# Performance work log

Hardware: AMD Instinct MI355X
Metric: run time of the kernel (lower is better)

The kernel has to match this reference:

```python
import jax, jax.numpy as jnp
import numpy as np

NUM_ROUTES, NUM_TIME, DIM, K, C = 100000, 2016, 256, 100, 5
BATCH = 262144


def _xavier(key, shape):
    fan_in, fan_out = shape[0], shape[1]
    lim = np.sqrt(6.0 / (fan_in + fan_out))
    return jax.random.uniform(key, shape, jnp.float32, -lim, lim)


def setup_inputs() -> dict:
    key = jax.random.key(0)
    ks = jax.random.split(key, 9)
    route_idx = jax.random.randint(ks[0], (BATCH,), 0, NUM_ROUTES)
    time_idx = jax.random.randint(ks[1], (BATCH,), 0, NUM_TIME)
    route_table = _xavier(ks[2], (NUM_ROUTES, DIM))
    time_table = _xavier(ks[3], (NUM_TIME, DIM))
    w = _xavier(ks[4], (DIM, K))
    mode_a = _xavier(ks[5], (DIM, C))
    mode_b = _xavier(ks[6], (DIM, C))
    mode_bias = jnp.zeros((C, C), jnp.float32)
    fc_lim = 1.0 / np.sqrt(C * C + K)
    fc_w = jax.random.uniform(ks[7], (C * C + K, 1), jnp.float32, -fc_lim, fc_lim)
    fc_b = jax.random.uniform(ks[8], (1,), jnp.float32, -fc_lim, fc_lim)
    return {
        "route_idx": route_idx, "time_idx": time_idx,
        "route_table": route_table, "time_table": time_table,
        "w": w, "mode_a": mode_a, "mode_b": mode_b,
        "mode_bias": mode_bias, "fc_w": fc_w, "fc_b": fc_b,
    }


def reference(route_idx, time_idx, route_table, time_table, w, mode_a, mode_b, mode_bias, fc_w, fc_b):
    r = route_table[route_idx]            # [B, D]
    t = time_table[time_idx]              # [B, D]
    gcp = jax.nn.relu((r * t) @ w)        # [B, K]
    # einsum('ni,nj->nij') then contracting i with mode_a and j with mode_b
    # equals outer product of the two small projections (exact same math):
    ra = r @ mode_a                       # [B, C]
    tb = t @ mode_b                       # [B, C]
    inter = jax.nn.sigmoid(ra[:, :, None] * tb[:, None, :] + mode_bias)  # [B, C, C]
    feats = jnp.concatenate([gcp, inter.reshape(inter.shape[0], -1)], axis=1)  # [B, K + C*C]
    out = feats @ fc_w + fc_b             # [B, 1]
    return jnp.squeeze(out, axis=-1)      # [B]
```

## Files before the change

kernel.cpp:

```cpp
#include <hip/hip_runtime.h>
#include <stdint.h>

#define BATCH   262144
#define NROUTES 100000
#define NTIME   2016
#define DIM     256
#define KOUT    100
#define NTILES  7

typedef __attribute__((ext_vector_type(2))) float f32x2;
typedef __attribute__((ext_vector_type(4))) float f32x4;

#define WS_WFRAG_BYTES ((size_t)(NTILES * 8 * 64 * 8))
#define WS_RA_OFF   (WS_WFRAG_BYTES)
#define WS_TB_OFF   (WS_RA_OFF + (size_t)NROUTES * 32)
#define WS_RT8_OFF  (WS_TB_OFF + (size_t)NTIME * 32)
#define WS_TT8_OFF  (WS_RT8_OFF + (size_t)NROUTES * 256)
#define WS_NEED     (WS_TT8_OFF + (size_t)NTIME * 256)

template<int CTRL>
static __device__ __forceinline__ float dpp_add(float x) {
  int s = __builtin_amdgcn_update_dpp(0, __builtin_bit_cast(int, x), CTRL, 0xF, 0xF, true);
  return x + __builtin_bit_cast(float, s);
}
static __device__ __forceinline__ float wave_sum63(float x) {
  x = dpp_add<0x111>(x);
  x = dpp_add<0x112>(x);
  x = dpp_add<0x114>(x);
  x = dpp_add<0x118>(x);
  x = dpp_add<0x142>(x);
  x = dpp_add<0x143>(x);
  return x;
}
static __device__ __forceinline__ float sum16_all(float x) {
  x = dpp_add<0x0B1>(x);
  x = dpp_add<0x04E>(x);
  x = dpp_add<0x124>(x);
  x = dpp_add<0x128>(x);
  return x;
}
static __device__ __forceinline__ float sigm(float z) {
  return __builtin_amdgcn_rcpf(1.0f + __expf(-z));
}

template<int DO8>
__global__ __launch_bounds__(256) void prep_kernel(
    const float* __restrict__ route_table,
    const float* __restrict__ time_table,
    const float* __restrict__ w,
    const float* __restrict__ mode_a,
    const float* __restrict__ mode_b,
    uint8_t* __restrict__ ws)
{
  const int b   = blockIdx.x;
  const int tid = threadIdx.x;

  if (b < 14) {
    const int u = b * 256 + tid;
    const int lane = u & 63;
    const int frag = u >> 6;
    const int ks = frag / NTILES;
    const int nt = frag % NTILES;
    const int n  = nt * 16 + (lane & 15);
    const int k0 = ks * 32 + (lane >> 4) * 8;
    float v[8];
    #pragma unroll
    for (int j = 0; j < 8; ++j)
      v[j] = (n < KOUT) ? w[(size_t)(k0 + j) * KOUT + n] : 0.0f;
    uint32_t d0 = 0, d1 = 0;
    d0 = __builtin_amdgcn_cvt_pk_fp8_f32(v[0], v[1], d0, false);
    d0 = __builtin_amdgcn_cvt_pk_fp8_f32(v[2], v[3], d0, true);
    d1 = __builtin_amdgcn_cvt_pk_fp8_f32(v[4], v[5], d1, false);
    d1 = __builtin_amdgcn_cvt_pk_fp8_f32(v[6], v[7], d1, true);
    ((uint2*)ws)[u] = make_uint2(d0, d1);
    return;
  }

  const float* tab; const float* proj; float* outp; uint8_t* out8; int base;
  if (b < 14 + 63) {
    tab = time_table;  proj = mode_b; outp = (float*)(ws + WS_TB_OFF);
    out8 = ws + WS_TT8_OFF; base = (b - 14) * 32;
  } else {
    tab = route_table; proj = mode_a; outp = (float*)(ws + WS_RA_OFF);
    out8 = ws + WS_RT8_OFF; base = (b - 77) * 32;
  }

  const int wave = tid >> 6, lane = tid & 63;
  const int perm = (2 * (lane >> 4) + ((lane >> 1) & 1)) * 8 +
                   ((lane >> 2) & 3) * 2 + (lane & 1);

  float A[4][5];
  #pragma unroll
  for (int j = 0; j < 4; ++j)
    #pragma unroll
    for (int i = 0; i < 5; ++i)
      A[j][i] = proj[(4 * perm + j) * 5 + i];

  const int row0 = base + wave * 8;
  float4 v[8];
  #pragma unroll
  for (int rr = 0; rr < 8; ++rr)
    v[rr] = *(const float4*)(tab + (size_t)(row0 + rr) * DIM + 4 * perm);

  #pragma unroll
  for (int rr = 0; rr < 8; ++rr) {
    const int row = row0 + rr;
    if (DO8) {
      uint32_t u = 0;
      u = __builtin_amdgcn_cvt_pk_fp8_f32(8.f * v[rr].x, 8.f * v[rr].y, u, false);
      u = __builtin_amdgcn_cvt_pk_fp8_f32(8.f * v[rr].z, 8.f * v[rr].w, u, true);
      *(uint32_t*)(out8 + (size_t)row * 256 + 4 * lane) = u;
    }
    float p[5];
    #pragma unroll
    for (int i = 0; i < 5; ++i) {
      float s = v[rr].x * A[0][i] + v[rr].y * A[1][i] + v[rr].z * A[2][i] + v[rr].w * A[3][i];
      p[i] = wave_sum63(s);
    }
    if (lane == 63) {
      float* o = outp + (size_t)row * 8;
      *(f32x4*)o = (f32x4){p[0], p[1], p[2], p[3]};
      o[4] = p[4];
    }
  }
}

__global__ __launch_bounds__(256, 3) void main_pipelined(
    const int*   __restrict__ route_idx,
    const int*   __restrict__ time_idx,
    const float* __restrict__ mode_bias,
    const float* __restrict__ fc_w,
    const float* __restrict__ fc_b,
    const uint8_t* __restrict__ ws,
    float* __restrict__ out)
{
  __shared__ uint4 wlds[1792];
  const int tid  = threadIdx.x;
  const int wave = tid >> 6, lane = tid & 63;
  const int col  = lane & 15, quad = lane >> 4;
  const int base = (blockIdx.x * 4 + wave) * 64;

  int ri[4], ti[4];
  #pragma unroll
  for (int t = 0; t < 4; ++t) {
    ri[t] = route_idx[base + t * 16 + col];
    ti[t] = time_idx[base + t * 16 + col];
  }

  {
    const uint4* wsrc = (const uint4*)ws;
    #pragma unroll
    for (int j = 0; j < 7; ++j)
      wlds[j * 256 + tid] = wsrc[j * 256 + tid];
  }

  float fcw_l[NTILES];
  #pragma unroll
  for (int nt = 0; nt < NTILES; ++nt) {
    const int n = nt * 16 + col;
    fcw_l[nt] = (n < KOUT) ? fc_w[n] * 0.015625f : 0.0f;
  }
  const float fb = fc_b[0];

  uint4 rw[2][4], tw[2][4];
  auto issue = [&](int buf, int t) {
    const uint8_t* rb = ws + WS_RT8_OFF + (size_t)ri[t] * 256 + quad * 16;
    const uint8_t* tb = ws + WS_TT8_OFF + (size_t)ti[t] * 256 + quad * 16;
    #pragma unroll
    for (int i = 0; i < 4; ++i) {
      rw[buf][i] = *(const uint4*)(rb + i * 64);
      tw[buf][i] = *(const uint4*)(tb + i * 64);
    }
  };

  issue(0, 0);
  __syncthreads();

  const uint2* wl2 = (const uint2*)wlds;

  #pragma unroll
  for (int it = 0; it < 4; ++it) {
    const int cb = it & 1, nb = cb ^ 1;

    const float* rap = (const float*)(ws + WS_RA_OFF) + (size_t)ri[it] * 8;
    const float* tbp = (const float*)(ws + WS_TB_OFF) + (size_t)ti[it] * 8;
    f32x4 ra0 = *(const f32x4*)rap; float ra4 = rap[4];
    f32x4 tb0 = *(const f32x4*)tbp; float tb4 = tbp[4];
    if (it < 3) issue(nb, it + 1);

    f32x4 acc[NTILES];
    #pragma unroll
    for (int nt = 0; nt < NTILES; ++nt) acc[nt] = (f32x4){0.f, 0.f, 0.f, 0.f};

    #pragma unroll
    for (int ks = 0; ks < 8; ++ks) {
      const int i = ks >> 1;
      const uint32_t ra = (ks & 1) ? rw[cb][i].z : rw[cb][i].x;
      const uint32_t rb = (ks & 1) ? rw[cb][i].w : rw[cb][i].y;
      const uint32_t ta = (ks & 1) ? tw[cb][i].z : tw[cb][i].x;
      const uint32_t tb = (ks & 1) ? tw[cb][i].w : tw[cb][i].y;
      f32x2 r01 = __builtin_amdgcn_cvt_pk_f32_fp8(ra, false);
      f32x2 r23 = __builtin_amdgcn_cvt_pk_f32_fp8(ra, true);
      f32x2 r45 = __builtin_amdgcn_cvt_pk_f32_fp8(rb, false);
      f32x2 r67 = __builtin_amdgcn_cvt_pk_f32_fp8(rb, true);
      f32x2 t01 = __builtin_amdgcn_cvt_pk_f32_fp8(ta, false);
      f32x2 t23 = __builtin_amdgcn_cvt_pk_f32_fp8(ta, true);
      f32x2 t45 = __builtin_amdgcn_cvt_pk_f32_fp8(tb, false);
      f32x2 t67 = __builtin_amdgcn_cvt_pk_f32_fp8(tb, true);
      f32x2 x01 = r01 * t01, x23 = r23 * t23, x45 = r45 * t45, x67 = r67 * t67;
      uint32_t p0 = 0, p1 = 0;
      p0 = __builtin_amdgcn_cvt_pk_fp8_f32(x01.x, x01.y, p0, false);
      p0 = __builtin_amdgcn_cvt_pk_fp8_f32(x23.x, x23.y, p0, true);
      p1 = __builtin_amdgcn_cvt_pk_fp8_f32(x45.x, x45.y, p1, false);
      p1 = __builtin_amdgcn_cvt_pk_fp8_f32(x67.x, x67.y, p1, true);
      const long a64 = __builtin_bit_cast(long, make_uint2(p0, p1));
      #pragma unroll
      for (int nt = 0; nt < NTILES; ++nt) {
        const long b64 = __builtin_bit_cast(long, wl2[(ks * NTILES + nt) * 64 + lane]);
        acc[nt] = __builtin_amdgcn_mfma_f32_16x16x32_fp8_fp8(a64, b64, acc[nt], 0, 0, 0);
      }
    }

    float s[4];
    #pragma unroll
    for (int reg = 0; reg < 4; ++reg) {
      float v = 0.f;
      #pragma unroll
      for (int nt = 0; nt < NTILES; ++nt)
        v += fmaxf(acc[nt][reg], 0.f) * fcw_l[nt];
      s[reg] = sum16_all(v);
    }

    const float rav[5] = {ra0.x, ra0.y, ra0.z, ra0.w, ra4};
    const float tbv[5] = {tb0.x, tb0.y, tb0.z, tb0.w, tb4};
    const float rq = (quad & 2) ? ((quad & 1) ? rav[3] : rav[2])
                                : ((quad & 1) ? rav[1] : rav[0]);
    const float tq = (quad & 2) ? ((quad & 1) ? tbv[3] : tbv[2])
                                : ((quad & 1) ? tbv[1] : tbv[0]);
    float sig = 0.f;
    #pragma unroll
    for (int j = 0; j < 5; ++j)
      sig += sigm(rq * tbv[j] + mode_bias[5 * quad + j]) * fc_w[KOUT + 5 * quad + j];
    sig += sigm(rav[4] * tq + mode_bias[20 + quad]) * fc_w[KOUT + 20 + quad];
    if (quad == 0)
      sig += sigm(rav[4] * tbv[4] + mode_bias[24]) * fc_w[KOUT + 24];
    sig += __shfl_xor(sig, 16, 64);
    sig += __shfl_xor(sig, 32, 64);

    if (quad == (col >> 2)) {
      const float sa = (col & 1) ? s[1] : s[0];
      const float sb = (col & 1) ? s[3] : s[2];
      const float gcp = (col & 2) ? sb : sa;
      out[base + it * 16 + col] = fb + gcp + sig;
    }
  }
}

__global__ __launch_bounds__(256, 4) void main_fallback(
    const int*   __restrict__ route_idx,
    const int*   __restrict__ time_idx,
    const float* __restrict__ route_table,
    const float* __restrict__ time_table,
    const float* __restrict__ mode_bias,
    const float* __restrict__ fc_w,
    const float* __restrict__ fc_b,
    const uint8_t* __restrict__ ws,
    float* __restrict__ out)
{
  __shared__ uint4 wlds[1792];
  const int tid  = threadIdx.x;
  const int wave = tid >> 6, lane = tid & 63;
  const int col  = lane & 15, quad = lane >> 4;
  const int m0   = blockIdx.x * 64 + wave * 16;
  const size_t ri = (size_t)route_idx[m0 + col];
  const size_t ti = (size_t)time_idx[m0 + col];

  const float* rap = (const float*)(ws + WS_RA_OFF) + ri * 8;
  const float* tbp = (const float*)(ws + WS_TB_OFF) + ti * 8;
  f32x4 ra0 = *(const f32x4*)rap; float ra4 = rap[4];
  f32x4 tb0 = *(const f32x4*)tbp; float tb4 = tbp[4];

  {
    const uint4* wsrc = (const uint4*)ws;
    #pragma unroll
    for (int j = 0; j < 7; ++j)
      wlds[j * 256 + tid] = wsrc[j * 256 + tid];
  }
  __syncthreads();

  float fcw_l[NTILES];
  #pragma unroll
  for (int nt = 0; nt < NTILES; ++nt) {
    const int n = nt * 16 + col;
    fcw_l[nt] = (n < KOUT) ? fc_w[n] * 0.015625f : 0.0f;
  }

  f32x4 acc[NTILES];
  #pragma unroll
  for (int nt = 0; nt < NTILES; ++nt) acc[nt] = (f32x4){0.f, 0.f, 0.f, 0.f};
  const uint2* wl2 = (const uint2*)wlds;

  #pragma unroll
  for (int ks = 0; ks < 8; ++ks) {
    const float4* rp = (const float4*)(route_table + ri * DIM + ks * 32 + quad * 8);
    const float4* tp = (const float4*)(time_table  + ti * DIM + ks * 32 + quad * 8);
    float4 r0 = rp[0], r1 = rp[1], t0 = tp[0], t1 = tp[1];
    uint32_t p0 = 0, p1 = 0;
    p0 = __builtin_amdgcn_cvt_pk_fp8_f32(64.f * r0.x * t0.x, 64.f * r0.y * t0.y, p0, false);
    p0 = __builtin_amdgcn_cvt_pk_fp8_f32(64.f * r0.z * t0.z, 64.f * r0.w * t0.w, p0, true);
    p1 = __builtin_amdgcn_cvt_pk_fp8_f32(64.f * r1.x * t1.x, 64.f * r1.y * t1.y, p1, false);
    p1 = __builtin_amdgcn_cvt_pk_fp8_f32(64.f * r1.z * t1.z, 64.f * r1.w * t1.w, p1, true);
    const long a64 = __builtin_bit_cast(long, make_uint2(p0, p1));
    #pragma unroll
    for (int nt = 0; nt < NTILES; ++nt) {
      const long b64 = __builtin_bit_cast(long, wl2[(ks * NTILES + nt) * 64 + lane]);
      acc[nt] = __builtin_amdgcn_mfma_f32_16x16x32_fp8_fp8(a64, b64, acc[nt], 0, 0, 0);
    }
  }

  float s[4];
  #pragma unroll
  for (int reg = 0; reg < 4; ++reg) {
    float v = 0.f;
    #pragma unroll
    for (int nt = 0; nt < NTILES; ++nt)
      v += fmaxf(acc[nt][reg], 0.f) * fcw_l[nt];
    s[reg] = sum16_all(v);
  }

  const float rav[5] = {ra0.x, ra0.y, ra0.z, ra0.w, ra4};
  const float tbv[5] = {tb0.x, tb0.y, tb0.z, tb0.w, tb4};
  const float rq = (quad & 2) ? ((quad & 1) ? rav[3] : rav[2])
                              : ((quad & 1) ? rav[1] : rav[0]);
  const float tq = (quad & 2) ? ((quad & 1) ? tbv[3] : tbv[2])
                              : ((quad & 1) ? tbv[1] : tbv[0]);
  float sig = 0.f;
  #pragma unroll
  for (int j = 0; j < 5; ++j)
    sig += sigm(rq * tbv[j] + mode_bias[5 * quad + j]) * fc_w[KOUT + 5 * quad + j];
  sig += sigm(rav[4] * tq + mode_bias[20 + quad]) * fc_w[KOUT + 20 + quad];
  if (quad == 0)
    sig += sigm(rav[4] * tbv[4] + mode_bias[24]) * fc_w[KOUT + 24];
  sig += __shfl_xor(sig, 16, 64);
  sig += __shfl_xor(sig, 32, 64);

  if (quad == (col >> 2)) {
    const float sa = (col & 1) ? s[1] : s[0];
    const float sb = (col & 1) ? s[3] : s[2];
    const float gcp = (col & 2) ? sb : sa;
    out[m0 + col] = fc_b[0] + gcp + sig;
  }
}

extern "C" void kernel_launch(void* const* d_in, const int* in_sizes, int n_in,
                              void* d_out, int out_size, void* d_ws, size_t ws_size,
                              hipStream_t stream)
{
  const int*   route_idx   = (const int*)d_in[0];
  const int*   time_idx    = (const int*)d_in[1];
  const float* route_table = (const float*)d_in[2];
  const float* time_table  = (const float*)d_in[3];
  const float* w           = (const float*)d_in[4];
  const float* mode_a      = (const float*)d_in[5];
  const float* mode_b      = (const float*)d_in[6];
  const float* mode_bias   = (const float*)d_in[7];
  const float* fc_w        = (const float*)d_in[8];
  const float* fc_b        = (const float*)d_in[9];
  uint8_t* ws  = (uint8_t*)d_ws;
  float*   out = (float*)d_out;

  const int big = (ws_size >= WS_NEED) ? 1 : 0;

  if (big) {
    prep_kernel<1><<<3202, 256, 0, stream>>>(route_table, time_table, w,
                                             mode_a, mode_b, ws);
    main_pipelined<<<BATCH / 256, 256, 0, stream>>>(route_idx, time_idx,
                                                    mode_bias, fc_w, fc_b, ws, out);
  } else {
    prep_kernel<0><<<3202, 256, 0, stream>>>(route_table, time_table, w,
                                             mode_a, mode_b, ws);
    main_fallback<<<BATCH / 64, 256, 0, stream>>>(route_idx, time_idx,
                                                  route_table, time_table,
                                                  mode_bias, fc_w, fc_b, ws, out);
  }
}
```

Measured before the change: 202.5 us.

## Make main kernel persistent with per-wave tile ranges and rolling prefetch

Replaces the one-block-per-256-rows launch with a persistent grid of 768 blocks. Each wave processes 5 or 6 consecutive 16-row tiles and double-buffers the fp8 row gathers and index loads one tile ahead. Mode bias and fc weights for the sigmoid term are hoisted into registers. This cuts block launch overhead and the repeated LDS weight staging per block, and keeps gathers in flight across tiles, at the cost of more register pressure and less load balancing.

Result: slower. 249.1 us (+23.0%).

```diff
diff --git a/kernel.cpp b/kernel.cpp
--- a/kernel.cpp
+++ b/kernel.cpp
@@ -125,7 +125,7 @@
   }
 }
 
-__global__ __launch_bounds__(256, 3) void main_pipelined(
+__global__ __launch_bounds__(256, 3) void main_persistent(
     const int*   __restrict__ route_idx,
     const int*   __restrict__ time_idx,
     const float* __restrict__ mode_bias,
@@ -138,14 +138,10 @@
   const int tid  = threadIdx.x;
   const int wave = tid >> 6, lane = tid & 63;
   const int col  = lane & 15, quad = lane >> 4;
-  const int base = (blockIdx.x * 4 + wave) * 64;
-
-  int ri[4], ti[4];
-  #pragma unroll
-  for (int t = 0; t < 4; ++t) {
-    ri[t] = route_idx[base + t * 16 + col];
-    ti[t] = time_idx[base + t * 16 + col];
-  }
+
+  const int wid = blockIdx.x * 4 + wave;
+  const int cnt = 5 + ((wid % 3) == 0 ? 1 : 0);
+  const int g0  = 5 * wid + (wid + 2) / 3;
 
   {
     const uint4* wsrc = (const uint4*)ws;
@@ -162,32 +158,33 @@
   }
   const float fb = fc_b[0];
 
-  uint4 rw[2][4], tw[2][4];
-  auto issue = [&](int buf, int t) {
-    const uint8_t* rb = ws + WS_RT8_OFF + (size_t)ri[t] * 256 + quad * 16;
-    const uint8_t* tb = ws + WS_TT8_OFF + (size_t)ti[t] * 256 + quad * 16;
+  float bias_q[5], fcs_q[5];
+  #pragma unroll
+  for (int j = 0; j < 5; ++j) {
+    bias_q[j] = mode_bias[5 * quad + j];
+    fcs_q[j]  = fc_w[KOUT + 5 * quad + j];
+  }
+  const float bias20 = mode_bias[20 + quad];
+  const float fcs20  = fc_w[KOUT + 20 + quad];
+  const float bias24 = mode_bias[24];
+  const float fcs24  = fc_w[KOUT + 24];
+
+  uint4 rw0[4], tw0[4], rw1[4], tw1[4];
+
+  auto issue = [&](uint4 (&rw)[4], uint4 (&tw)[4], int ri, int ti) {
+    const uint8_t* rb = ws + WS_RT8_OFF + (size_t)ri * 256 + quad * 16;
+    const uint8_t* tb = ws + WS_TT8_OFF + (size_t)ti * 256 + quad * 16;
     #pragma unroll
     for (int i = 0; i < 4; ++i) {
-      rw[buf][i] = *(const uint4*)(rb + i * 64);
-      tw[buf][i] = *(const uint4*)(tb + i * 64);
+      rw[i] = *(const uint4*)(rb + i * 64);
+      tw[i] = *(const uint4*)(tb + i * 64);
     }
   };
 
-  issue(0, 0);
-  __syncthreads();
-
   const uint2* wl2 = (const uint2*)wlds;
 
-  #pragma unroll
-  for (int it = 0; it < 4; ++it) {
-    const int cb = it & 1, nb = cb ^ 1;
-
-    const float* rap = (const float*)(ws + WS_RA_OFF) + (size_t)ri[it] * 8;
-    const float* tbp = (const float*)(ws + WS_TB_OFF) + (size_t)ti[it] * 8;
-    f32x4 ra0 = *(const f32x4*)rap; float ra4 = rap[4];
-    f32x4 tb0 = *(const f32x4*)tbp; float tb4 = tbp[4];
-    if (it < 3) issue(nb, it + 1);
-
+  auto compute = [&](const uint4 (&rwb)[4], const uint4 (&twb)[4],
+                     f32x4 raV, float raV4, f32x4 tbV, float tbV4, int T) {
     f32x4 acc[NTILES];
     #pragma unroll
     for (int nt = 0; nt < NTILES; ++nt) acc[nt] = (f32x4){0.f, 0.f, 0.f, 0.f};
@@ -195,10 +192,10 @@
     #pragma unroll
     for (int ks = 0; ks < 8; ++ks) {
       const int i = ks >> 1;
-      const uint32_t ra = (ks & 1) ? rw[cb][i].z : rw[cb][i].x;
-      const uint32_t rb = (ks & 1) ? rw[cb][i].w : rw[cb][i].y;
-      const uint32_t ta = (ks & 1) ? tw[cb][i].z : tw[cb][i].x;
-      const uint32_t tb = (ks & 1) ? tw[cb][i].w : tw[cb][i].y;
+      const uint32_t ra = (ks & 1) ? rwb[i].z : rwb[i].x;
+      const uint32_t rb = (ks & 1) ? rwb[i].w : rwb[i].y;
+      const uint32_t ta = (ks & 1) ? twb[i].z : twb[i].x;
+      const uint32_t tb = (ks & 1) ? twb[i].w : twb[i].y;
       f32x2 r01 = __builtin_amdgcn_cvt_pk_f32_fp8(ra, false);
       f32x2 r23 = __builtin_amdgcn_cvt_pk_f32_fp8(ra, true);
       f32x2 r45 = __builtin_amdgcn_cvt_pk_f32_fp8(rb, false);
@@ -231,8 +228,8 @@
       s[reg] = sum16_all(v);
     }
 
-    const float rav[5] = {ra0.x, ra0.y, ra0.z, ra0.w, ra4};
-    const float tbv[5] = {tb0.x, tb0.y, tb0.z, tb0.w, tb4};
+    const float rav[5] = {raV.x, raV.y, raV.z, raV.w, raV4};
+    const float tbv[5] = {tbV.x, tbV.y, tbV.z, tbV.w, tbV4};
     const float rq = (quad & 2) ? ((quad & 1) ? rav[3] : rav[2])
                                 : ((quad & 1) ? rav[1] : rav[0]);
     const float tq = (quad & 2) ? ((quad & 1) ? tbv[3] : tbv[2])
@@ -240,10 +237,10 @@
     float sig = 0.f;
     #pragma unroll
     for (int j = 0; j < 5; ++j)
-      sig += sigm(rq * tbv[j] + mode_bias[5 * quad + j]) * fc_w[KOUT + 5 * quad + j];
-    sig += sigm(rav[4] * tq + mode_bias[20 + quad]) * fc_w[KOUT + 20 + quad];
+      sig += sigm(rq * tbv[j] + bias_q[j]) * fcs_q[j];
+    sig += sigm(rav[4] * tq + bias20) * fcs20;
     if (quad == 0)
-      sig += sigm(rav[4] * tbv[4] + mode_bias[24]) * fc_w[KOUT + 24];
+      sig += sigm(rav[4] * tbv[4] + bias24) * fcs24;
     sig += __shfl_xor(sig, 16, 64);
     sig += __shfl_xor(sig, 32, 64);
 
@@ -251,8 +248,45 @@
       const float sa = (col & 1) ? s[1] : s[0];
       const float sb = (col & 1) ? s[3] : s[2];
       const float gcp = (col & 2) ? sb : sa;
-      out[base + it * 16 + col] = fb + gcp + sig;
-    }
+      out[T * 16 + col] = fb + gcp + sig;
+    }
+  };
+
+  int riA = route_idx[g0 * 16 + col];
+  int tiA = time_idx[g0 * 16 + col];
+  issue(rw0, tw0, riA, tiA);
+  int riB = route_idx[(g0 + 1) * 16 + col];
+  int tiB = time_idx[(g0 + 1) * 16 + col];
+  __syncthreads();
+
+  int it = 0;
+  while (true) {
+    {
+      const float* rap = (const float*)(ws + WS_RA_OFF) + (size_t)riA * 8;
+      const float* tbp = (const float*)(ws + WS_TB_OFF) + (size_t)tiA * 8;
+      f32x4 raV = *(const f32x4*)rap; float raV4 = rap[4];
+      f32x4 tbV = *(const f32x4*)tbp; float tbV4 = tbp[4];
+      if (it + 1 < cnt) issue(rw1, tw1, riB, tiB);
+      if (it + 2 < cnt) {
+        riA = route_idx[(g0 + it + 2) * 16 + col];
+        tiA = time_idx[(g0 + it + 2) * 16 + col];
+      }
+      compute(rw0, tw0, raV, raV4, tbV, tbV4, g0 + it);
+    }
+    ++it; if (it == cnt) break;
+    {
+      const float* rap = (const float*)(ws + WS_RA_OFF) + (size_t)riB * 8;
+      const float* tbp = (const float*)(ws + WS_TB_OFF) + (size_t)tiB * 8;
+      f32x4 raV = *(const f32x4*)rap; float raV4 = rap[4];
+      f32x4 tbV = *(const f32x4*)tbp; float tbV4 = tbp[4];
+      if (it + 1 < cnt) issue(rw0, tw0, riA, tiA);
+      if (it + 2 < cnt) {
+        riB = route_idx[(g0 + it + 2) * 16 + col];
+        tiB = time_idx[(g0 + it + 2) * 16 + col];
+      }
+      compute(rw1, tw1, raV, raV4, tbV, tbV4, g0 + it);
+    }
+    ++it; if (it == cnt) break;
   }
 }
 
@@ -374,8 +408,8 @@
   if (big) {
     prep_kernel<1><<<3202, 256, 0, stream>>>(route_table, time_table, w,
                                              mode_a, mode_b, ws);
-    main_pipelined<<<BATCH / 256, 256, 0, stream>>>(route_idx, time_idx,
-                                                    mode_bias, fc_w, fc_b, ws, out);
+    main_persistent<<<768, 256, 0, stream>>>(route_idx, time_idx,
+                                             mode_bias, fc_w, fc_b, ws, out);
   } else {
     prep_kernel<0><<<3202, 256, 0, stream>>>(route_table, time_table, w,
                                              mode_a, mode_b, ws);
```
